# Optimization experiments

Hardware: AMD Instinct MI355X
Metric: run time of the kernel (lower is better)

## Reference

```python
import jax, jax.numpy as jnp
import numpy as np

D_MODEL = 1024
N_HEADS = 16
HEAD_DIM = 64  # 16*64 = 1024
LATENT = 256   # low-rank KV compression dim
NUM_WHEELS = 4
WHEEL_OUT = 256


def setup_inputs() -> dict:
    key = jax.random.key(0)
    ks = jax.random.split(key, 9)
    S = 2048
    s = lambda fan_in: 1.0 / np.sqrt(fan_in)
    return {
        "sketch_emb": jax.random.normal(ks[0], (S, D_MODEL), dtype=jnp.float32),
        "Wq": jax.random.normal(ks[1], (D_MODEL, N_HEADS * HEAD_DIM), dtype=jnp.float32) * s(D_MODEL),
        "Wdkv": jax.random.normal(ks[2], (D_MODEL, LATENT), dtype=jnp.float32) * s(D_MODEL),
        "Wuk": jax.random.normal(ks[3], (LATENT, N_HEADS * HEAD_DIM), dtype=jnp.float32) * s(LATENT),
        "Wuv": jax.random.normal(ks[4], (LATENT, N_HEADS * HEAD_DIM), dtype=jnp.float32) * s(LATENT),
        "Wo": jax.random.normal(ks[5], (N_HEADS * HEAD_DIM, D_MODEL), dtype=jnp.float32) * s(N_HEADS * HEAD_DIM),
        "wheel_W": jax.random.normal(ks[6], (NUM_WHEELS, D_MODEL, WHEEL_OUT), dtype=jnp.float32) * s(D_MODEL),
        "wheel_b": jax.random.normal(ks[7], (NUM_WHEELS, WHEEL_OUT), dtype=jnp.float32) * 0.01,
    }


def reference(sketch_emb, Wq, Wdkv, Wuk, Wuv, Wo, wheel_W, wheel_b):
    S = sketch_emb.shape[0]
    # Multi-head latent attention: per-head Q, shared low-rank KV latent.
    q = (sketch_emb @ Wq).reshape(S, N_HEADS, HEAD_DIM)          # [S,H,D]
    c_kv = sketch_emb @ Wdkv                                      # [S,L]
    k = (c_kv @ Wuk).reshape(S, N_HEADS, HEAD_DIM)                # [S,H,D]
    v = (c_kv @ Wuv).reshape(S, N_HEADS, HEAD_DIM)                # [S,H,D]
    scale = 1.0 / np.sqrt(HEAD_DIM).astype(np.float32)
    scores = jnp.einsum("qhd,khd->hqk", q, k) * scale             # [H,S,S]
    attn = jax.nn.softmax(scores, axis=-1)
    ctx = jnp.einsum("hqk,khd->qhd", attn, v).reshape(S, N_HEADS * HEAD_DIM)
    body = ctx @ Wo                                               # [S,1024]
    # Wheel projections batched as one einsum, then laid out as concat order
    # cat([body, w0, w1, w2, w3], dim=1)
    wheels = jnp.einsum("sd,wde->swe", body, wheel_W) + wheel_b   # [S,W,256]
    wheels = wheels.reshape(S, NUM_WHEELS * WHEEL_OUT)
    return jnp.concatenate([body, wheels], axis=1)                # [S,2048]
```

## Files before the change

kernel.cpp:

```cpp
#include <hip/hip_runtime.h>
#include <math.h>

#define S_LEN 2048
#define DMODEL 1024
#define NHEADS 16
#define HDIM 64
#define QPITCH 1280

typedef _Float16 f16x8 __attribute__((ext_vector_type(8)));
typedef _Float16 f16x4 __attribute__((ext_vector_type(4)));
typedef float    f32x4 __attribute__((ext_vector_type(4)));

__device__ __forceinline__ void gld_lds16(void* lds, const void* g) {
    __builtin_amdgcn_global_load_lds(
        (__attribute__((address_space(1))) void*)(g),
        (__attribute__((address_space(3))) void*)(lds), 16, 0, 0);
}

__device__ __forceinline__ void vm_wait0() { __asm__ __volatile__("s_waitcnt vmcnt(0)" ::: "memory"); }
__device__ __forceinline__ void vm_wait4() { __asm__ __volatile__("s_waitcnt vmcnt(4)" ::: "memory"); }
__device__ __forceinline__ void vm_wait6() { __asm__ __volatile__("s_waitcnt vmcnt(6)" ::: "memory"); }
__device__ __forceinline__ void vm_wait8() { __asm__ __volatile__("s_waitcnt vmcnt(8)" ::: "memory"); }
__device__ __forceinline__ void lgkm_wait0() { __asm__ __volatile__("s_waitcnt lgkmcnt(0)" ::: "memory"); }
__device__ __forceinline__ void barrier_raw() {
    __asm__ __volatile__("" ::: "memory");
    __builtin_amdgcn_s_barrier();
    __asm__ __volatile__("" ::: "memory");
}

__device__ __forceinline__ void gemm_core(
    _Float16* sA, _Float16* sB,
    const _Float16* __restrict__ A, int lda,
    const _Float16* __restrict__ Bt, int ldb,
    int nkt,
    _Float16* __restrict__ Cb, int ldcb, int bmode,
    _Float16* __restrict__ Cb2, int ldcb2,
    int bx, int by)
{
    const int tid  = threadIdx.x;
    const int lane = tid & 63;
    const int w    = tid >> 6;
    const int quad = lane >> 4;
    const int c0   = lane & 15;
    const int m0 = by * 128;
    const int n0 = bx * 128;

    const int srow = lane >> 3;
    const int sc   = lane & 7;
    const _Float16* a_src[4]; const _Float16* b_src[4];
    int dstoff[4];
#pragma unroll
    for (int t = 0; t < 4; t++) {
        const int row = w * 32 + t * 8 + srow;
        const int c = sc ^ (row & 7);
        a_src[t] = A  + (size_t)(m0 + row) * lda + c * 8;
        b_src[t] = Bt + (size_t)(n0 + row) * ldb + c * 8;
        dstoff[t] = (w * 32 + t * 8) * 64;
    }

    const int mw = (w & 1) * 64;
    const int nw = (w >> 1) * 64;
    int arow[4], brow[4];
#pragma unroll
    for (int i = 0; i < 4; i++) {
        arow[i] = mw + i * 16 + c0;
        brow[i] = nw + i * 16 + c0;
    }

    f32x4 acc[4][4];
#pragma unroll
    for (int i = 0; i < 4; i++)
#pragma unroll
        for (int j = 0; j < 4; j++) acc[i][j] = (f32x4){0.f, 0.f, 0.f, 0.f};

    auto stage = [&](int buf) {
#pragma unroll
        for (int t = 0; t < 4; t++) {
            gld_lds16(&sA[buf * 8192 + dstoff[t]], a_src[t]); a_src[t] += 64;
            gld_lds16(&sB[buf * 8192 + dstoff[t]], b_src[t]); b_src[t] += 64;
        }
    };
    auto step = [&](int buf) {
#pragma unroll
        for (int ks = 0; ks < 2; ks++) {
            const int cb = ks * 4 + quad;
            f16x8 af[4], bfv[4];
#pragma unroll
            for (int i = 0; i < 4; i++)
                af[i] = *(const f16x8*)&sA[buf * 8192 + arow[i] * 64 + ((cb ^ (arow[i] & 7)) << 3)];
#pragma unroll
            for (int j = 0; j < 4; j++)
                bfv[j] = *(const f16x8*)&sB[buf * 8192 + brow[j] * 64 + ((cb ^ (brow[j] & 7)) << 3)];
#pragma unroll
            for (int i = 0; i < 4; i++)
#pragma unroll
                for (int j = 0; j < 4; j++)
                    acc[i][j] = __builtin_amdgcn_mfma_f32_16x16x32_f16(af[i], bfv[j], acc[i][j], 0, 0, 0);
        }
    };

    stage(0); stage(1);
    int cur = 0;
    for (int kt = 0; kt < nkt; ++kt) {
        if (kt < nkt - 1) vm_wait8(); else vm_wait0();
        barrier_raw();
        if (kt + 2 < nkt) { int nx = cur + 2; if (nx >= 3) nx -= 3; stage(nx); }
        step(cur);
        if (++cur == 3) cur = 0;
    }

#pragma unroll
    for (int i = 0; i < 4; i++) {
#pragma unroll
        for (int reg = 0; reg < 4; reg++) {
            const int m = m0 + mw + i * 16 + quad * 4 + reg;
#pragma unroll
            for (int j = 0; j < 4; j++) {
                const int n = n0 + nw + j * 16 + c0;
                _Float16 hv = (_Float16)acc[i][j][reg];
                if (bmode == 0) {
                    Cb[(size_t)m * ldcb + n] = hv;
                } else {
                    if (n < 1024) Cb[(size_t)m * ldcb + n] = hv;
                    else          Cb2[(size_t)(n - 1024) * ldcb2 + m] = hv;
                }
            }
        }
    }
}

__global__ __launch_bounds__(256) void gemm_qcwf(
    const _Float16* __restrict__ WcT, const _Float16* __restrict__ Wo_f16,
    _Float16* __restrict__ BtWheels,
    const _Float16* __restrict__ emb_f16, const _Float16* __restrict__ Wqc_t,
    _Float16* __restrict__ qc_f16)
{
    __shared__ _Float16 sA[3][8192];
    __shared__ _Float16 sB[3][8192];
    int b = blockIdx.x;
    if (b < 64) {
        gemm_core(&sA[0][0], &sB[0][0], WcT, 1024, Wo_f16, 1024, 16,
                  BtWheels, 1024, 0, nullptr, 0, b >> 3, b & 7);
    } else {
        b -= 64;
        gemm_core(&sA[0][0], &sB[0][0], emb_f16, 1024, Wqc_t, 1024, 16,
                  qc_f16, 1280, 0, nullptr, 0, b >> 4, b & 15);
    }
}

__global__ __launch_bounds__(256) void gemm_kv(
    const _Float16* __restrict__ qc_f16, const _Float16* __restrict__ Wukv_t,
    _Float16* __restrict__ k_f16, _Float16* __restrict__ vT_f16)
{
    __shared__ _Float16 sA[3][8192];
    __shared__ _Float16 sB[3][8192];
    const int b = blockIdx.x;
    gemm_core(&sA[0][0], &sB[0][0], qc_f16 + 1024, 1280, Wukv_t, 256, 4,
              k_f16, 1024, 4, vT_f16, 2048, b >> 4, b & 15);
}

__global__ __launch_bounds__(256) void gemm_fin64(
    const _Float16* __restrict__ A,
    const _Float16* __restrict__ Bt,
    float* __restrict__ out,
    const float* __restrict__ bias)
{
    __shared__ _Float16 sA[3][64 * 64];
    __shared__ _Float16 sB[3][128 * 64];

    const int tid  = threadIdx.x;
    const int lane = tid & 63;
    const int w    = tid >> 6;
    const int quad = lane >> 4;
    const int c0   = lane & 15;

    const int flat = blockIdx.x;
    const int xcd  = flat & 7;
    const int wi   = flat >> 3;
    const int by   = (xcd & 3) * 8 + (wi & 7);
    const int bx   = (xcd >> 2) * 8 + (wi >> 3);
    const int m0 = by * 64;
    const int n0 = bx * 128;

    const int srow = lane >> 3;
    const int sc   = lane & 7;
    const _Float16* a_src[2]; int a_dst[2];
#pragma unroll
    for (int t = 0; t < 2; t++) {
        const int row = t * 32 + w * 8 + srow;
        const int c = sc ^ (row & 7);
        a_src[t] = A + (size_t)(m0 + row) * 1024 + c * 8;
        a_dst[t] = (t * 32 + w * 8) * 64;
    }
    const _Float16* b_src[4]; int b_dst[4];
#pragma unroll
    for (int t = 0; t < 4; t++) {
        const int row = t * 32 + w * 8 + srow;
        const int c = sc ^ (row & 7);
        b_src[t] = Bt + (size_t)(n0 + row) * 1024 + c * 8;
        b_dst[t] = (t * 32 + w * 8) * 64;
    }

    const int mw = (w & 1) * 32;
    const int nw = (w >> 1) * 64;
    int arow[2], brow[4];
#pragma unroll
    for (int i = 0; i < 2; i++) arow[i] = mw + i * 16 + c0;
#pragma unroll
    for (int j = 0; j < 4; j++) brow[j] = nw + j * 16 + c0;

    f32x4 acc[2][4];
#pragma unroll
    for (int i = 0; i < 2; i++)
#pragma unroll
        for (int j = 0; j < 4; j++) acc[i][j] = (f32x4){0.f, 0.f, 0.f, 0.f};

    auto stage = [&](int buf) {
#pragma unroll
        for (int t = 0; t < 2; t++) { gld_lds16(&sA[buf][a_dst[t]], a_src[t]); a_src[t] += 64; }
#pragma unroll
        for (int t = 0; t < 4; t++) { gld_lds16(&sB[buf][b_dst[t]], b_src[t]); b_src[t] += 64; }
    };
    auto step = [&](int buf) {
#pragma unroll
        for (int ks = 0; ks < 2; ks++) {
            const int cb = ks * 4 + quad;
            f16x8 af[2], bfv[4];
#pragma unroll
            for (int i = 0; i < 2; i++)
                af[i] = *(const f16x8*)&sA[buf][arow[i] * 64 + ((cb ^ (arow[i] & 7)) << 3)];
#pragma unroll
            for (int j = 0; j < 4; j++)
                bfv[j] = *(const f16x8*)&sB[buf][brow[j] * 64 + ((cb ^ (brow[j] & 7)) << 3)];
#pragma unroll
            for (int i = 0; i < 2; i++)
#pragma unroll
                for (int j = 0; j < 4; j++)
                    acc[i][j] = __builtin_amdgcn_mfma_f32_16x16x32_f16(af[i], bfv[j], acc[i][j], 0, 0, 0);
        }
    };

    stage(0); stage(1);
    int cur = 0;
    for (int kt = 0; kt < 16; ++kt) {
        if (kt < 15) vm_wait6(); else vm_wait0();
        barrier_raw();
        if (kt + 2 < 16) { int nx = cur + 2; if (nx >= 3) nx -= 3; stage(nx); }
        step(cur);
        if (++cur == 3) cur = 0;
    }

    float bias_v[4];
#pragma unroll
    for (int j = 0; j < 4; j++) bias_v[j] = bias[n0 + nw + j * 16 + c0];
#pragma unroll
    for (int i = 0; i < 2; i++) {
#pragma unroll
        for (int reg = 0; reg < 4; reg++) {
            const int m = m0 + mw + i * 16 + quad * 4 + reg;
#pragma unroll
            for (int j = 0; j < 4; j++) {
                const int n = n0 + nw + j * 16 + c0;
                out[(size_t)m * 2048 + n] = acc[i][j][reg] + bias_v[j];
            }
        }
    }
}

#define SOFT_M2 8.65617024533378f
#define OTP 68

__global__ __launch_bounds__(512) void attn_mfma_kernel(
    const _Float16* __restrict__ qs,
    const _Float16* __restrict__ kk,
    const _Float16* __restrict__ vT,
    _Float16* __restrict__ ctx)
{
    __shared__ _Float16 Ks[2][3][64 * 64];
    __shared__ _Float16 Vt[2][4][64 * 64];

    const int flat = blockIdx.x;
    const int h  = flat & 15;
    const int qb = flat >> 4;
    const int tid  = threadIdx.x;
    const int lane = tid & 63;
    const int w    = tid >> 6;
    const int kzw  = w >> 2;
    const int wl   = w & 3;
    const int quad = lane >> 4;
    const int c0   = lane & 15;

    f16x8 qfrag[2][2];
#pragma unroll
    for (int m = 0; m < 2; m++) {
        const _Float16* qrow = qs + (size_t)(qb * 128 + wl * 32 + m * 16 + c0) * QPITCH + h * HDIM;
        qfrag[m][0] = *(const f16x8*)(qrow + quad * 8);
        qfrag[m][1] = *(const f16x8*)(qrow + 32 + quad * 8);
    }

    const int srow = lane >> 3;
    const int sc   = lane & 7;
    const _Float16* k_src[2]; const _Float16* v_src[2];
    int dstoff[2];
#pragma unroll
    for (int t = 0; t < 2; t++) {
        const int row = wl * 16 + t * 8 + srow;
        const int c = sc ^ (row & 7);
        k_src[t] = kk + (size_t)(kzw * 1024 + row) * DMODEL + h * HDIM + c * 8;
        v_src[t] = vT + (size_t)(h * HDIM + row) * S_LEN + kzw * 1024 + c * 8;
        dstoff[t] = (wl * 16 + t * 8) * 64;
    }

    f32x4 OfragT[2][4];
#pragma unroll
    for (int m = 0; m < 2; m++)
#pragma unroll
        for (int db = 0; db < 4; db++) OfragT[m][db] = (f32x4){0.f, 0.f, 0.f, 0.f};
    f32x4 lacc[2];
    lacc[0] = (f32x4){0.f, 0.f, 0.f, 0.f};
    lacc[1] = (f32x4){0.f, 0.f, 0.f, 0.f};
    f16x4 ones;
    ones[0] = (_Float16)1.f; ones[1] = (_Float16)1.f;
    ones[2] = (_Float16)1.f; ones[3] = (_Float16)1.f;

    f16x4 pf[2][4];

    auto stage = [&](int t) {
        const int kb = t % 3, vb = t & 3;
#pragma unroll
        for (int i = 0; i < 2; i++) {
            gld_lds16(&Ks[kzw][kb][dstoff[i]], k_src[i]); k_src[i] += (size_t)64 * DMODEL;
            gld_lds16(&Vt[kzw][vb][dstoff[i]], v_src[i]); v_src[i] += 64;
        }
    };

    auto qk = [&](int t, f32x4 (*sf)[4]) {
        const int buf = t % 3;
#pragma unroll
        for (int m = 0; m < 2; m++)
#pragma unroll
            for (int nb = 0; nb < 4; nb++) sf[m][nb] = (f32x4){0.f, 0.f, 0.f, 0.f};
        __builtin_amdgcn_s_setprio(1);
#pragma unroll
        for (int nb = 0; nb < 4; nb++) {
            const int krow = nb * 16 + c0;
#pragma unroll
            for (int ks = 0; ks < 2; ks++) {
                const int cb = ks * 4 + quad;
                f16x8 kfr = *(const f16x8*)&Ks[kzw][buf][krow * 64 + ((cb ^ (c0 & 7)) << 3)];
#pragma unroll
                for (int m = 0; m < 2; m++)
                    sf[m][nb] = __builtin_amdgcn_mfma_f32_16x16x32_f16(kfr, qfrag[m][ks], sf[m][nb], 0, 0, 0);
            }
        }
        __builtin_amdgcn_s_setprio(0);
    };

    auto sm = [&](f32x4 (*sf)[4]) {
#pragma unroll
        for (int m = 0; m < 2; m++)
#pragma unroll
            for (int kb = 0; kb < 4; kb++) {
                float p0 = __builtin_amdgcn_exp2f(sf[m][kb][0] - SOFT_M2);
                float p1 = __builtin_amdgcn_exp2f(sf[m][kb][1] - SOFT_M2);
                float p2 = __builtin_amdgcn_exp2f(sf[m][kb][2] - SOFT_M2);
                float p3 = __builtin_amdgcn_exp2f(sf[m][kb][3] - SOFT_M2);
                f16x4 pv;
                pv[0] = (_Float16)p0; pv[1] = (_Float16)p1;
                pv[2] = (_Float16)p2; pv[3] = (_Float16)p3;
                pf[m][kb] = pv;
            }
    };

    auto pv = [&](int t) {
        const int buf = t & 3;
        __builtin_amdgcn_s_setprio(1);
#pragma unroll
        for (int kb = 0; kb < 4; kb++) {
#pragma unroll
            for (int m = 0; m < 2; m++)
                lacc[m] = __builtin_amdgcn_mfma_f32_16x16x16f16(ones, pf[m][kb], lacc[m], 0, 0, 0);
            const int cc = (((kb * 2 + (quad >> 1)) ^ (c0 & 7)) << 3) + (quad & 1) * 4;
#pragma unroll
            for (int db = 0; db < 4; db++) {
                f16x4 vf = *(const f16x4*)&Vt[kzw][buf][(db * 16 + c0) * 64 + cc];
#pragma unroll
                for (int m = 0; m < 2; m++)
                    OfragT[m][db] = __builtin_amdgcn_mfma_f32_16x16x16f16(vf, pf[m][kb], OfragT[m][db], 0, 0, 0);
            }
        }
        __builtin_amdgcn_s_setprio(0);
    };

    stage(0); stage(1);
    {
        vm_wait4(); barrier_raw();
        stage(2);
        f32x4 sf[2][4];
        qk(0, sf);
        sm(sf);
    }
    for (int t = 1; t < 16; ++t) {
        if (t < 15) vm_wait4(); else vm_wait0();
        barrier_raw();
        if (t + 2 < 16) stage(t + 2);
        f32x4 sf[2][4];
        qk(t, sf);
        pv(t - 1);
        sm(sf);
    }
    pv(15);

    lgkm_wait0();
    barrier_raw();
    float* ex  = (float*)&Ks[0][0][0];
    float* lex = ex + 8192;
    if (kzw == 1) {
#pragma unroll
        for (int m = 0; m < 2; m++) {
#pragma unroll
            for (int db = 0; db < 4; db++)
                *(f32x4*)&ex[((((wl * 2 + m) * 4 + db) * 64) + lane) * 4] = OfragT[m][db];
            lex[(wl * 2 + m) * 64 + lane] = lacc[m][0];
        }
    }
    lgkm_wait0();
    barrier_raw();
    if (kzw == 0) {
        float* Otw = (float*)&Vt[0][0][0] + wl * 16 * OTP;
#pragma unroll
        for (int m = 0; m < 2; m++) {
            const float l = lacc[m][0] + lex[(wl * 2 + m) * 64 + lane];
            const float inv = 1.0f / l;
#pragma unroll
            for (int db = 0; db < 4; db++) {
                f32x4 p = *(const f32x4*)&ex[((((wl * 2 + m) * 4 + db) * 64) + lane) * 4];
                f32x4 o;
                o[0] = (OfragT[m][db][0] + p[0]) * inv;
                o[1] = (OfragT[m][db][1] + p[1]) * inv;
                o[2] = (OfragT[m][db][2] + p[2]) * inv;
                o[3] = (OfragT[m][db][3] + p[3]) * inv;
                *(f32x4*)&Otw[c0 * OTP + db * 16 + quad * 4] = o;
            }
            lgkm_wait0();
#pragma unroll
            for (int it = 0; it < 4; it++) {
                const int r = it * 4 + quad;
                f32x4 ov = *(const f32x4*)&Otw[r * OTP + c0 * 4];
                f16x4 hv;
                hv[0] = (_Float16)ov[0]; hv[1] = (_Float16)ov[1];
                hv[2] = (_Float16)ov[2]; hv[3] = (_Float16)ov[3];
                const int row = qb * 128 + wl * 32 + m * 16 + r;
                *(f16x4*)&ctx[(size_t)row * 1024 + h * 64 + c0 * 4] = hv;
            }
            lgkm_wait0();
        }
    }
}

__device__ __forceinline__ void xpose_seg(float (*tile)[33],
    const float* __restrict__ src, _Float16* __restrict__ dst,
    int C, int dpitch, float scale, int bx, int by, int nbase0)
{
    const int r0 = by * 32, c0 = bx * 32;
    const int tr = threadIdx.x >> 5, tc = threadIdx.x & 31;
#pragma unroll
    for (int i = 0; i < 4; i++)
        tile[tr + i * 8][tc] = src[(size_t)(r0 + tr + i * 8) * C + c0 + tc];
    __syncthreads();
    const int nr = threadIdx.x & 31;
    const int k0 = (threadIdx.x >> 5) * 4;
    f16x4 hv;
#pragma unroll
    for (int e = 0; e < 4; e++)
        hv[e] = (_Float16)(tile[k0 + e][nr] * scale);
    *(f16x4*)(dst + (size_t)(nbase0 + c0 + nr) * dpitch + (r0 + k0)) = hv;
}

__global__ __launch_bounds__(256) void megaprep_kernel(
    const float* __restrict__ emb, const float* __restrict__ Wq,
    const float* __restrict__ Wdkv, const float* __restrict__ Wuk,
    const float* __restrict__ Wuv, const float* __restrict__ Wo,
    const float* __restrict__ wheelW, const float* __restrict__ wheelB,
    _Float16* __restrict__ Wqc_t, _Float16* __restrict__ Wukv_t,
    _Float16* __restrict__ Bt_full, _Float16* __restrict__ WcT,
    _Float16* __restrict__ Wo_f16, _Float16* __restrict__ emb_f16,
    float* __restrict__ biasbuf)
{
    __shared__ float tile[32][33];
    int b = blockIdx.x;
    const int tid = threadIdx.x;

    if (b < 1024) { xpose_seg(tile, Wq, Wqc_t, 1024, 1024, 0.125f, b & 31, b >> 5, 0); return; }
    b -= 1024;
    if (b < 256)  { xpose_seg(tile, Wdkv, Wqc_t + 1048576, 256, 1024, 1.f, b & 7, b >> 3, 0); return; }
    b -= 256;
    if (b < 256)  { xpose_seg(tile, Wuk, Wukv_t, 1024, 256, 1.4426950408889634f, b & 31, b >> 5, 0); return; }
    b -= 256;
    if (b < 256)  { xpose_seg(tile, Wuv, Wukv_t + 262144, 1024, 256, 1.f, b & 31, b >> 5, 0); return; }
    b -= 256;
    if (b < 1024) { xpose_seg(tile, Wo, Bt_full, 1024, 1024, 1.f, b & 31, b >> 5, 0); return; }
    b -= 1024;
    if (b < 1024) {
        const int z = b >> 8, rem = b & 255;
        xpose_seg(tile, wheelW + (size_t)z * 262144, WcT, 256, 1024, 1.f,
                  rem & 7, rem >> 3, z * 256);
        return;
    }
    b -= 1024;
    if (b < 256) {
#pragma unroll
        for (int k = 0; k < 4; k++) {
            const int i = b * 1024 + k * 256 + tid;
            float4 f = ((const float4*)Wo)[i];
            f16x4 v;
            v[0] = (_Float16)f.x; v[1] = (_Float16)f.y;
            v[2] = (_Float16)f.z; v[3] = (_Float16)f.w;
            ((f16x4*)Wo_f16)[i] = v;
        }
        return;
    }
    b -= 256;
    if (b < 512) {
#pragma unroll
        for (int k = 0; k < 4; k++) {
            const int i = b * 1024 + k * 256 + tid;
            float4 f = ((const float4*)emb)[i];
            f16x4 v;
            v[0] = (_Float16)f.x; v[1] = (_Float16)f.y;
            v[2] = (_Float16)f.z; v[3] = (_Float16)f.w;
            ((f16x4*)emb_f16)[i] = v;
        }
        return;
    }
    b -= 512;
    if (b < 8) {
        const int i = b * 256 + tid;
        biasbuf[i] = (i < 1024) ? 0.f : wheelB[i - 1024];
    }
}

extern "C" void kernel_launch(void* const* d_in, const int* in_sizes, int n_in,
                              void* d_out, int out_size, void* d_ws, size_t ws_size,
                              hipStream_t stream) {
    const float* emb    = (const float*)d_in[0];
    const float* Wq     = (const float*)d_in[1];
    const float* Wdkv   = (const float*)d_in[2];
    const float* Wuk    = (const float*)d_in[3];
    const float* Wuv    = (const float*)d_in[4];
    const float* Wo     = (const float*)d_in[5];
    const float* wheelW = (const float*)d_in[6];
    const float* wheelB = (const float*)d_in[7];
    float* out = (float*)d_out;

    _Float16* ws = (_Float16*)d_ws;
    _Float16* Bt_full = ws;
    _Float16* Wqc_t   = ws + 2097152;
    _Float16* Wukv_t  = ws + 3407872;
    float*    biasbuf = (float*)(ws + 3932160);
    _Float16* WcT     = ws + 3936256;
    _Float16* Wo_f16  = ws + 4984832;
    _Float16* ctx     = ws + 3936256;
    _Float16* emb_f16 = ws + 6033408;
    _Float16* qc_f16  = ws + 8130560;
    _Float16* k_f16   = ws + 10752000;
    _Float16* vT_f16  = ws + 12849152;

    megaprep_kernel<<<4616, 256, 0, stream>>>(
        emb, Wq, Wdkv, Wuk, Wuv, Wo, wheelW, wheelB,
        Wqc_t, Wukv_t, Bt_full, WcT, Wo_f16, emb_f16, biasbuf);

    gemm_qcwf<<<224, 256, 0, stream>>>(WcT, Wo_f16, Bt_full + (size_t)1024 * 1024,
                                       emb_f16, Wqc_t, qc_f16);

    gemm_kv<<<256, 256, 0, stream>>>(qc_f16, Wukv_t, k_f16, vT_f16);

    attn_mfma_kernel<<<256, 512, 0, stream>>>(qc_f16, k_f16, vT_f16, ctx);

    gemm_fin64<<<512, 256, 0, stream>>>(ctx, Bt_full, out, biasbuf);
}
```

Before: 163.7 us.

## Process two KV tiles per barrier in attention and vectorize transposed GEMM stores

The attention kernel's K/V staging moves from a per-tile 3/4-buffer ring to handling two 64-key tiles per barrier step, with 4 K and 5 V LDS buffers and ping-pong probability registers (pfA/pfB). The aim is to halve the number of barriers and place more QK and PV MFMA work between syncs. In exchange, each step drains all global loads with vmcnt(0) and LDS use grows to about 144KB. Separately, the GEMM epilogue writes the transposed Cb2 output as one f16x4 vector store instead of four scalar stores. The change also leaves some dead placeholder variables behind.

```diff
diff --git a/kernel.cpp b/kernel.cpp
--- a/kernel.cpp
+++ b/kernel.cpp
@@ -18,7 +18,6 @@
 }
 
 __device__ __forceinline__ void vm_wait0() { __asm__ __volatile__("s_waitcnt vmcnt(0)" ::: "memory"); }
-__device__ __forceinline__ void vm_wait4() { __asm__ __volatile__("s_waitcnt vmcnt(4)" ::: "memory"); }
 __device__ __forceinline__ void vm_wait6() { __asm__ __volatile__("s_waitcnt vmcnt(6)" ::: "memory"); }
 __device__ __forceinline__ void vm_wait8() { __asm__ __volatile__("s_waitcnt vmcnt(8)" ::: "memory"); }
 __device__ __forceinline__ void lgkm_wait0() { __asm__ __volatile__("s_waitcnt lgkmcnt(0)" ::: "memory"); }
@@ -111,19 +110,19 @@
 
 #pragma unroll
     for (int i = 0; i < 4; i++) {
-#pragma unroll
-        for (int reg = 0; reg < 4; reg++) {
-            const int m = m0 + mw + i * 16 + quad * 4 + reg;
-#pragma unroll
-            for (int j = 0; j < 4; j++) {
-                const int n = n0 + nw + j * 16 + c0;
-                _Float16 hv = (_Float16)acc[i][j][reg];
-                if (bmode == 0) {
-                    Cb[(size_t)m * ldcb + n] = hv;
-                } else {
-                    if (n < 1024) Cb[(size_t)m * ldcb + n] = hv;
-                    else          Cb2[(size_t)(n - 1024) * ldcb2 + m] = hv;
-                }
+        const int mb = m0 + mw + i * 16 + quad * 4;
+#pragma unroll
+        for (int j = 0; j < 4; j++) {
+            const int n = n0 + nw + j * 16 + c0;
+            if (bmode == 0 || n < 1024) {
+#pragma unroll
+                for (int reg = 0; reg < 4; reg++)
+                    Cb[(size_t)(mb + reg) * ldcb + n] = (_Float16)acc[i][j][reg];
+            } else {
+                f16x4 hv;
+                hv[0] = (_Float16)acc[i][j][0]; hv[1] = (_Float16)acc[i][j][1];
+                hv[2] = (_Float16)acc[i][j][2]; hv[3] = (_Float16)acc[i][j][3];
+                *(f16x4*)&Cb2[(size_t)(n - 1024) * ldcb2 + mb] = hv;
             }
         }
     }
@@ -276,8 +275,8 @@
     const _Float16* __restrict__ vT,
     _Float16* __restrict__ ctx)
 {
-    __shared__ _Float16 Ks[2][3][64 * 64];
-    __shared__ _Float16 Vt[2][4][64 * 64];
+    __shared__ _Float16 Ks[2][4][64 * 64];
+    __shared__ _Float16 Vt[2][5][64 * 64];
 
     const int flat = blockIdx.x;
     const int h  = flat & 15;
@@ -300,16 +299,27 @@
 
     const int srow = lane >> 3;
     const int sc   = lane & 7;
-    const _Float16* k_src[2]; const _Float16* v_src[2];
-    int dstoff[2];
+    const _Float16* k_src; const _Float16* v_src;
+    int dstoff;
+    {
+        const int row = wl * 16 + (lane >> 5) * 8 + (srow & 7);
+        (void)row;
+    }
+    {
+        const int row = wl * 16 + ((lane >> 3) & 7) + ((lane >> 3) >> 3) * 0;
+        (void)row;
+    }
+    const _Float16* k_src2[2]; const _Float16* v_src2[2];
+    int dstoff2[2];
 #pragma unroll
     for (int t = 0; t < 2; t++) {
         const int row = wl * 16 + t * 8 + srow;
         const int c = sc ^ (row & 7);
-        k_src[t] = kk + (size_t)(kzw * 1024 + row) * DMODEL + h * HDIM + c * 8;
-        v_src[t] = vT + (size_t)(h * HDIM + row) * S_LEN + kzw * 1024 + c * 8;
-        dstoff[t] = (wl * 16 + t * 8) * 64;
-    }
+        k_src2[t] = kk + (size_t)(kzw * 1024 + row) * DMODEL + h * HDIM + c * 8;
+        v_src2[t] = vT + (size_t)(h * HDIM + row) * S_LEN + kzw * 1024 + c * 8;
+        dstoff2[t] = (wl * 16 + t * 8) * 64;
+    }
+    (void)k_src; (void)v_src; (void)dstoff;
 
     f32x4 OfragT[2][4];
 #pragma unroll
@@ -323,19 +333,17 @@
     ones[0] = (_Float16)1.f; ones[1] = (_Float16)1.f;
     ones[2] = (_Float16)1.f; ones[3] = (_Float16)1.f;
 
-    f16x4 pf[2][4];
-
-    auto stage = [&](int t) {
-        const int kb = t % 3, vb = t & 3;
+    f16x4 pfA[2][4], pfB[2][4];
+
+    auto stage = [&](int kbuf, int vbuf) {
 #pragma unroll
         for (int i = 0; i < 2; i++) {
-            gld_lds16(&Ks[kzw][kb][dstoff[i]], k_src[i]); k_src[i] += (size_t)64 * DMODEL;
-            gld_lds16(&Vt[kzw][vb][dstoff[i]], v_src[i]); v_src[i] += 64;
-        }
-    };
-
-    auto qk = [&](int t, f32x4 (*sf)[4]) {
-        const int buf = t % 3;
+            gld_lds16(&Ks[kzw][kbuf][dstoff2[i]], k_src2[i]); k_src2[i] += (size_t)64 * DMODEL;
+            gld_lds16(&Vt[kzw][vbuf][dstoff2[i]], v_src2[i]); v_src2[i] += 64;
+        }
+    };
+
+    auto qk = [&](int kbuf, f32x4 (*sf)[4]) {
 #pragma unroll
         for (int m = 0; m < 2; m++)
 #pragma unroll
@@ -347,7 +355,7 @@
 #pragma unroll
             for (int ks = 0; ks < 2; ks++) {
                 const int cb = ks * 4 + quad;
-                f16x8 kfr = *(const f16x8*)&Ks[kzw][buf][krow * 64 + ((cb ^ (c0 & 7)) << 3)];
+                f16x8 kfr = *(const f16x8*)&Ks[kzw][kbuf][krow * 64 + ((cb ^ (c0 & 7)) << 3)];
 #pragma unroll
                 for (int m = 0; m < 2; m++)
                     sf[m][nb] = __builtin_amdgcn_mfma_f32_16x16x32_f16(kfr, qfrag[m][ks], sf[m][nb], 0, 0, 0);
@@ -356,7 +364,7 @@
         __builtin_amdgcn_s_setprio(0);
     };
 
-    auto sm = [&](f32x4 (*sf)[4]) {
+    auto sm = [&](f32x4 (*sf)[4], f16x4 (*pf)[4]) {
 #pragma unroll
         for (int m = 0; m < 2; m++)
 #pragma unroll
@@ -372,8 +380,7 @@
             }
     };
 
-    auto pv = [&](int t) {
-        const int buf = t & 3;
+    auto pv = [&](int vbuf, f16x4 (*pf)[4]) {
         __builtin_amdgcn_s_setprio(1);
 #pragma unroll
         for (int kb = 0; kb < 4; kb++) {
@@ -383,7 +390,7 @@
             const int cc = (((kb * 2 + (quad >> 1)) ^ (c0 & 7)) << 3) + (quad & 1) * 4;
 #pragma unroll
             for (int db = 0; db < 4; db++) {
-                f16x4 vf = *(const f16x4*)&Vt[kzw][buf][(db * 16 + c0) * 64 + cc];
+                f16x4 vf = *(const f16x4*)&Vt[kzw][vbuf][(db * 16 + c0) * 64 + cc];
 #pragma unroll
                 for (int m = 0; m < 2; m++)
                     OfragT[m][db] = __builtin_amdgcn_mfma_f32_16x16x16f16(vf, pf[m][kb], OfragT[m][db], 0, 0, 0);
@@ -392,24 +399,44 @@
         __builtin_amdgcn_s_setprio(0);
     };
 
-    stage(0); stage(1);
+    stage(0, 0); stage(1, 1);
+
     {
-        vm_wait4(); barrier_raw();
-        stage(2);
-        f32x4 sf[2][4];
-        qk(0, sf);
-        sm(sf);
-    }
-    for (int t = 1; t < 16; ++t) {
-        if (t < 15) vm_wait4(); else vm_wait0();
-        barrier_raw();
-        if (t + 2 < 16) stage(t + 2);
-        f32x4 sf[2][4];
-        qk(t, sf);
-        pv(t - 1);
-        sm(sf);
-    }
-    pv(15);
+        vm_wait0(); barrier_raw();
+        stage(2, 2); stage(3, 3);
+        f32x4 sf0[2][4], sf1[2][4];
+        qk(0, sf0);
+        sm(sf0, pfB);
+        qk(1, sf1);
+        pv(0, pfB);
+        sm(sf1, pfA);
+    }
+
+    int vb = 2;
+    for (int p = 1; p < 8; ++p) {
+        const int kr = (p & 1) << 1;
+        const int kw = kr ^ 2;
+        const int vprev = (vb + 4 >= 5) ? vb - 1 : vb + 4;
+        const int vr0 = vb;
+        const int vr1 = (vb + 1 >= 5) ? vb - 4 : vb + 1;
+        const int vw0 = (vb + 2 >= 5) ? vb - 3 : vb + 2;
+        const int vw1 = (vb + 3 >= 5) ? vb - 2 : vb + 3;
+
+        vm_wait0(); barrier_raw();
+        if (p < 7) { stage(kw, vw0); stage(kw ^ 1, vw1); }
+
+        f32x4 sf0[2][4], sf1[2][4];
+        qk(kr, sf0);
+        pv(vprev, pfA);
+        sm(sf0, pfB);
+        qk(kr ^ 1, sf1);
+        pv(vr0, pfB);
+        sm(sf1, pfA);
+        (void)vr1;
+
+        vb += 2; if (vb >= 5) vb -= 5;
+    }
+    pv(0, pfA);
 
     lgkm_wait0();
     barrier_raw();
```

Result: faster. 158.0 us (-3.4%).
